# Optimization experiments

Measured on AMD Instinct MI355X. Metric: run time of the kernel, lower is better.

The kernel has to match this reference:

```python
import jax, jax.numpy as jnp
import numpy as np
from jax.scipy.special import gammaln

B, N, F, K = 128, 29, 64, 64
MAXZ, NITER, NPATH = 56, 2, 20
CUTOFF = 5.0


def setup_inputs() -> dict:
    key = jax.random.key(0)
    ks = jax.random.split(key, 16)
    atomic_numbers = jax.random.randint(ks[0], (B, N), 1, MAXZ)
    positions = jax.random.normal(ks[1], (B, N, 3), dtype=jnp.float32) * 2.0
    Ef = jax.random.normal(ks[2], (B, 3), dtype=jnp.float32)
    # fully connected molecular graph (all ordered pairs i != j), E = N*(N-1) = 812
    ii, jj = np.meshgrid(np.arange(N), np.arange(N), indexing="ij")
    m = ii != jj
    dst_idx = jnp.asarray(ii[m], dtype=jnp.int32)
    src_idx = jnp.asarray(jj[m], dtype=jnp.int32)
    s = 1.0 / np.sqrt(F)
    t = 0.2  # tensor-product path weight scale (keeps activations bounded)
    return {
        "atomic_numbers": atomic_numbers, "positions": positions, "Ef": Ef,
        "dst_idx": dst_idx, "src_idx": src_idx,
        "embed": jax.random.normal(ks[3], (MAXZ, F), dtype=jnp.float32) * s,
        "mp_basis_w": jax.random.normal(ks[4], (NITER, K, F), dtype=jnp.float32) / np.sqrt(K),
        "mp_tp_w": jax.random.normal(ks[5], (NITER, NPATH, F), dtype=jnp.float32) * t,
        "d1_w": jax.random.normal(ks[6], (NITER, 2, 2, F, F), dtype=jnp.float32) * s,
        "d1_b": jnp.zeros((NITER, 2, F), dtype=jnp.float32),
        "d2_w": jax.random.normal(ks[7], (NITER, 2, 2, F, F), dtype=jnp.float32) * s,
        "d2_b": jnp.zeros((NITER, 2, F), dtype=jnp.float32),
        "tens_w": jax.random.normal(ks[8], (NITER, NPATH, F), dtype=jnp.float32) * t,
        "td_dense_w": jax.random.normal(ks[9], (NITER, 2, 2, F, F), dtype=jnp.float32) * s,
        "td_tp_w": jax.random.normal(ks[10], (NITER, NPATH, F), dtype=jnp.float32) * t,
        "out_w": jax.random.normal(ks[11], (F,), dtype=jnp.float32) * s,
        "element_bias": jax.random.normal(ks[12], (MAXZ,), dtype=jnp.float32) * 0.1,
    }


def _tp(a, b, w):
    """Channelwise Clebsch-Gordan tensor product for max_degree=1 with parity channels.
    a, b: (M, 2, 4, F) with axis1 = (regular, pseudo), axis2 = (l=0, l=1 x/y/z).
    w: (20, F) learned per-path weights (5 l-paths x 4 parity combos)."""
    M, Fd = a.shape[0], a.shape[-1]
    sr = jnp.zeros((M, Fd), a.dtype); sp = jnp.zeros((M, Fd), a.dtype)
    vr = jnp.zeros((M, 3, Fd), a.dtype); vp = jnp.zeros((M, 3, Fd), a.dtype)
    idx = 0
    for p1 in range(2):
        for p2 in range(2):
            s1 = a[:, p1, 0]; v1 = a[:, p1, 1:4]
            s2 = b[:, p2, 0]; v2 = b[:, p2, 1:4]
            pl0a = 1 - 2 * p1; pl0b = 1 - 2 * p2   # parity of l=0 slot
            pl1a = -(1 - 2 * p1); pl1b = -(1 - 2 * p2)  # parity of l=1 slot
            tt = w[idx] * s1 * s2
            if pl0a * pl0b == 1: sr = sr + tt
            else: sp = sp + tt
            tt = w[idx + 1] * s1[:, None, :] * v2
            if pl0a * pl1b == -1: vr = vr + tt
            else: vp = vp + tt
            tt = w[idx + 2] * v1 * s2[:, None, :]
            if pl1a * pl0b == -1: vr = vr + tt
            else: vp = vp + tt
            tt = w[idx + 3] * jnp.sum(v1 * v2, axis=1)
            if pl1a * pl1b == 1: sr = sr + tt
            else: sp = sp + tt
            tt = w[idx + 4] * jnp.cross(v1, v2, axis=1)
            if pl1a * pl1b == -1: vr = vr + tt
            else: vp = vp + tt
            idx += 5
    reg = jnp.concatenate([sr[:, None, :], vr], axis=1)
    pse = jnp.concatenate([sp[:, None, :], vp], axis=1)
    return jnp.stack([reg, pse], axis=1)  # (M, 2, 4, F)


def _dense(x, W, b=None):
    # per-(parity, degree) linear map over features; W: (2, 2, F, F), b: (2, F)
    s = jnp.einsum("npf,pfg->npg", x[:, :, 0, :], W[:, 0])
    v = jnp.einsum("npdf,pfg->npdg", x[:, :, 1:4, :], W[:, 1])
    if b is not None:
        s = s + b
    return jnp.concatenate([s[:, :, None, :], v], axis=2)


def _silu(x):
    # gated equivariant silu: silu on scalars, sigmoid(scalar) gate on vectors
    s = x[:, :, 0:1, :]
    g = jax.nn.sigmoid(s)
    return jnp.concatenate([s * g, x[:, :, 1:4, :] * g], axis=2)


def _radial(r):
    # reciprocal Bernstein radial basis with smooth cutoff
    k = jnp.arange(K, dtype=r.dtype)
    logc = gammaln(float(K)) - gammaln(k + 1.0) - gammaln(float(K) - k)
    u = 1.0 / (1.0 + r)
    logb = logc + k * jnp.log(u)[:, None] + (K - 1.0 - k) * jnp.log(jnp.maximum(1.0 - u, 1e-12))[:, None]
    x2 = (r / CUTOFF) ** 2
    fcut = jnp.where(x2 < 1.0, jnp.exp(1.0 - 1.0 / jnp.maximum(1.0 - x2, 1e-12)), 0.0)
    return jnp.exp(logb) * fcut[:, None]  # (E, K)


def reference(atomic_numbers, positions, Ef, dst_idx, src_idx, embed, mp_basis_w,
              mp_tp_w, d1_w, d1_b, d2_w, d2_b, tens_w, td_dense_w, td_tp_w,
              out_w, element_bias):
    Bsz, Nn = atomic_numbers.shape
    BN = Bsz * Nn
    Fd = embed.shape[-1]
    pos = positions.reshape(-1, 3)
    Z = atomic_numbers.reshape(-1)
    offsets = (jnp.arange(Bsz, dtype=dst_idx.dtype) * Nn)
    dstf = (dst_idx[None, :] + offsets[:, None]).reshape(-1)  # (B*E,)
    srcf = (src_idx[None, :] + offsets[:, None]).reshape(-1)
    disp = pos[srcf] - pos[dstf]                               # (B*E, 3)
    r = jnp.sqrt(jnp.sum(disp * disp, axis=-1) + 1e-12)
    unit = disp / r[:, None]
    sph = jnp.concatenate([jnp.ones_like(r)[:, None], unit], axis=-1)  # (B*E, 4)
    basis = sph[:, :, None] * _radial(r)[:, None, :]           # (B*E, 4, K)

    x = jnp.zeros((BN, 2, 4, Fd), dtype=positions.dtype)
    x = x.at[:, 0, 0, :].set(embed[Z])

    xEFv = jnp.concatenate([jnp.ones((Bsz, 1), positions.dtype), Ef], axis=-1)  # (B, 4)
    xEF = jnp.repeat(xEFv, Nn, axis=0)                          # (BN, 4)
    xEF = jnp.broadcast_to(xEF[:, None, :, None], (BN, 2, 4, Fd))

    for i in range(NITER):
        bproj = jnp.einsum("edk,kf->edf", basis, mp_basis_w[i])  # (B*E, 4, F)
        bfeat = jnp.stack([bproj, jnp.zeros_like(bproj)], axis=1)  # (B*E, 2, 4, F)
        msg = _tp(x[srcf], bfeat, mp_tp_w[i])
        if i == NITER - 1:  # last iteration: max_degree=0 messages
            msg = msg * jnp.array([1.0, 0.0, 0.0, 0.0], msg.dtype)[None, None, :, None]
        y = jax.ops.segment_sum(msg, dstf, num_segments=BN)
        x = x + y
        h = _dense(x, d1_w[i], d1_b[i])
        h = _silu(h)
        h = _dense(h, d2_w[i], d2_b[i])
        x = h + y
        x = x + _tp(x, xEF, tens_w[i])          # Tensor()(x, xEF)
        x = _tp(x, _dense(x, td_dense_w[i]), td_tp_w[i])  # TensorDense

    s = x[:, 0, 0, :]  # degree-0 regular channel
    atomic_energies = s @ out_w + element_bias[Z]
    energy = atomic_energies.reshape(Bsz, Nn).sum(axis=1)
    return energy
```

## Files before the change

kernel.cpp:

```cpp
#include <hip/hip_runtime.h>

#define NB 128
#define NA 29
#define BN (NB*NA)
#define FD 64


__global__ void prep_kernel(const float* __restrict__ d1b,
                            const float* __restrict__ d2b,
                            const float* __restrict__ d2w,
                            float* __restrict__ logc, float* __restrict__ c4,
                            float* __restrict__ out)
{
  const int t = threadIdx.x;
  if (t < 64) {
    logc[t] = lgammaf(64.0f) - lgammaf((float)t + 1.0f) - lgammaf(64.0f - (float)t);
  } else if (t < 128) {
    const int g = t - 64;
    float acc = d2b[64 + g];
    for (int f = 0; f < 64; ++f) {
      const float v  = d1b[64 + f];
      const float sv = v / (1.0f + expf(-v));
      acc += d2w[2*4096 + f*64 + g] * sv;
    }
    c4[g] = acc;
  } else {
    out[t - 128] = 0.0f;
  }
}

template<bool LAST>
__global__ __launch_bounds__(256) void fmsg_kernel(
    const int*   __restrict__ Z,
    const float* __restrict__ pos,
    const float* __restrict__ src,
    const float* __restrict__ wtp,
    const float* __restrict__ Wb,
    const float* __restrict__ logc_tab,
    float* __restrict__ y)
{
  __shared__ float elu[28], el1mu[28], efc[28];
  __shared__ float us[28][3];
  __shared__ float rads[28][FD];
  __shared__ float emb_sh[NA][FD];
  __shared__ float yred[4][4][FD];
  const int bn = blockIdx.x, b = bn / NA, n = bn - b*NA;
  const int tid = threadIdx.x, lane = tid & 63, wv = tid >> 6;

  if (tid < 28) {
    const int jr = tid, j = jr + (jr >= n ? 1 : 0);
    const float dx = pos[(b*NA+j)*3+0] - pos[(b*NA+n)*3+0];
    const float dy = pos[(b*NA+j)*3+1] - pos[(b*NA+n)*3+1];
    const float dz = pos[(b*NA+j)*3+2] - pos[(b*NA+n)*3+2];
    const float r  = sqrtf(dx*dx + dy*dy + dz*dz + 1e-12f);
    const float ri = 1.0f / r;
    us[jr][0] = dx*ri; us[jr][1] = dy*ri; us[jr][2] = dz*ri;
    const float u  = 1.0f/(1.0f + r);
    elu[jr]   = logf(u);
    el1mu[jr] = logf(fmaxf(1.0f - u, 1e-12f));
    const float x2 = (r*0.2f)*(r*0.2f);
    efc[jr] = (x2 < 1.0f) ? expf(1.0f - 1.0f/fmaxf(1.0f - x2, 1e-12f)) : 0.0f;
  }
  if constexpr (!LAST) {
    for (int idx = tid; idx < NA*FD; idx += 256)
      emb_sh[idx>>6][idx&63] = src[Z[b*NA + (idx>>6)]*FD + (idx&63)];
  }
  const float kk   = (float)lane;
  const float logc = logc_tab[lane];
  __syncthreads();

  #pragma unroll
  for (int i = 0; i < 7; ++i) {
    const int e = wv*7 + i;
    rads[e][lane] = expf(logc + kk*elu[e] + (63.0f - kk)*el1mu[e]) * efc[e];
  }
  float wb[64];
  #pragma unroll
  for (int k = 0; k < 64; ++k) wb[k] = Wb[k*FD + lane];

  float y0 = 0.0f, y1 = 0.0f, y2 = 0.0f, y3 = 0.0f, y4 = 0.0f;
  const float wm0 = wtp[0*FD + lane];
  const float wm1 = LAST ? 0.0f : wtp[1*FD + lane];
  const float wm3 = LAST ? wtp[3*FD + lane]  : 0.0f;
  const float wm5 = LAST ? wtp[10*FD + lane] : 0.0f;
  const float wm8 = LAST ? wtp[13*FD + lane] : 0.0f;

  #pragma unroll
  for (int i = 0; i < 7; ++i) {
    const int jr = wv*7 + i;
    float a0 = 0.0f;
    #pragma unroll
    for (int k4 = 0; k4 < 16; ++k4) {
      const float4 rv = *(const float4*)&rads[jr][k4*4];
      a0 += wb[k4*4+0]*rv.x + wb[k4*4+1]*rv.y + wb[k4*4+2]*rv.z + wb[k4*4+3]*rv.w;
    }
    const int j = jr + (jr >= n ? 1 : 0);
    const float ux = us[jr][0], uy = us[jr][1], uz = us[jr][2];
    if constexpr (!LAST) {
      const float t0 = a0 * emb_sh[j][lane];
      y0 += wm0*t0;
      const float t1 = wm1*t0;
      y1 += t1*ux; y2 += t1*uy; y3 += t1*uz;
    } else {
      const float* xj = src + (size_t)(b*NA + j)*512 + lane;
      const float s1   = xj[0];
      const float dot1 = xj[64]*ux + xj[128]*uy + xj[192]*uz;
      const float s1p  = xj[256];
      const float dotp = xj[320]*ux + xj[384]*uy + xj[448]*uz;
      y0 += a0*(wm0*s1  + wm3*dot1);
      y4 += a0*(wm5*s1p + wm8*dotp);
    }
  }

  if constexpr (!LAST) {
    yred[wv][0][lane] = y0; yred[wv][1][lane] = y1;
    yred[wv][2][lane] = y2; yred[wv][3][lane] = y3;
  } else {
    yred[wv][0][lane] = y0; yred[wv][1][lane] = y4;
  }
  __syncthreads();
  if (wv == 0) {
    if constexpr (!LAST) {
      #pragma unroll
      for (int c = 0; c < 4; ++c) {
        const float s = yred[0][c][lane] + yred[1][c][lane]
                      + yred[2][c][lane] + yred[3][c][lane];
        y[(size_t)bn*256 + c*64 + lane] = s;
      }
    } else {
      const float s0 = yred[0][0][lane] + yred[1][0][lane]
                     + yred[2][0][lane] + yred[3][0][lane];
      const float s4 = yred[0][1][lane] + yred[1][1][lane]
                     + yred[2][1][lane] + yred[3][1][lane];
      y[(size_t)bn*512 + lane]       = s0;
      y[(size_t)bn*512 + 256 + lane] = s4;
    }
  }
}

__device__ __forceinline__ void tp20(const float* a, const float* bb,
                                     const float* w, float* o)
{
  #pragma unroll
  for (int p1 = 0; p1 < 2; ++p1) {
    #pragma unroll
    for (int p2 = 0; p2 < 2; ++p2) {
      const float* w5 = w + 5*(2*p1 + p2);
      const float s1 = a[p1*4+0], x1 = a[p1*4+1], y1 = a[p1*4+2], z1 = a[p1*4+3];
      const float s2 = bb[p2*4+0], x2 = bb[p2*4+1], y2 = bb[p2*4+2], z2 = bb[p2*4+3];
      const int so = (p1 == p2) ? 0 : 4;
      const int vo = 4 - so;
      o[so+0] += w5[0]*(s1*s2) + w5[3]*(x1*x2 + y1*y2 + z1*z2);
      o[so+1] += w5[1]*(s1*x2) + w5[2]*(x1*s2);
      o[so+2] += w5[1]*(s1*y2) + w5[2]*(y1*s2);
      o[so+3] += w5[1]*(s1*z2) + w5[2]*(z1*s2);
      o[vo+1] += w5[4]*(y1*z2 - z1*y2);
      o[vo+2] += w5[4]*(z1*x2 - x1*z2);
      o[vo+3] += w5[4]*(x1*y2 - y1*x2);
    }
  }
}

__device__ __forceinline__ void stage2(float* __restrict__ wst,
                                       const float* __restrict__ src, int tid)
{
  const float4* s = (const float4*)src;
  float4* d = (float4*)wst;
  #pragma unroll
  for (int i = 0; i < 8; ++i) d[tid + i*256] = s[tid + i*256];
}

__device__ __forceinline__ void denseP2(const float* __restrict__ wst,
                                        const float* __restrict__ rA,
                                        const float* __restrict__ rB,
                                        float bs, int g,
                                        float oA[4], float oB[4])
{
  float a0A = bs, a0B = bs;
  #pragma unroll
  for (int f4 = 0; f4 < 16; ++f4) {
    const float w0 = wst[(f4*4+0)*64+g], w1 = wst[(f4*4+1)*64+g];
    const float w2 = wst[(f4*4+2)*64+g], w3 = wst[(f4*4+3)*64+g];
    const float4 xA = *(const float4*)&rA[f4*4];
    const float4 xB = *(const float4*)&rB[f4*4];
    a0A += w0*xA.x + w1*xA.y + w2*xA.z + w3*xA.w;
    a0B += w0*xB.x + w1*xB.y + w2*xB.z + w3*xB.w;
  }
  oA[0] = a0A; oB[0] = a0B;
  float a1A = 0, a2A = 0, a3A = 0, a1B = 0, a2B = 0, a3B = 0;
  #pragma unroll
  for (int f4 = 0; f4 < 16; ++f4) {
    const float w0 = wst[4096+(f4*4+0)*64+g], w1 = wst[4096+(f4*4+1)*64+g];
    const float w2 = wst[4096+(f4*4+2)*64+g], w3 = wst[4096+(f4*4+3)*64+g];
    const float4 aA = *(const float4*)&rA[ 64+f4*4];
    const float4 bA = *(const float4*)&rA[128+f4*4];
    const float4 cA = *(const float4*)&rA[192+f4*4];
    const float4 aB = *(const float4*)&rB[ 64+f4*4];
    const float4 bB = *(const float4*)&rB[128+f4*4];
    const float4 cB = *(const float4*)&rB[192+f4*4];
    a1A += w0*aA.x + w1*aA.y + w2*aA.z + w3*aA.w;
    a2A += w0*bA.x + w1*bA.y + w2*bA.z + w3*bA.w;
    a3A += w0*cA.x + w1*cA.y + w2*cA.z + w3*cA.w;
    a1B += w0*aB.x + w1*aB.y + w2*aB.z + w3*aB.w;
    a2B += w0*bB.x + w1*bB.y + w2*bB.z + w3*bB.w;
    a3B += w0*cB.x + w1*cB.y + w2*cB.z + w3*cB.w;
  }
  oA[1] = a1A; oA[2] = a2A; oA[3] = a3A;
  oB[1] = a1B; oB[2] = a2B; oB[3] = a3B;
}

template<bool LAST>
__global__ __launch_bounds__(256) void node_kernel(
    const int*   __restrict__ Z,
    const float* __restrict__ embed,
    const float* __restrict__ Ef,
    const float* __restrict__ d1w, const float* __restrict__ d1b,
    const float* __restrict__ d2w, const float* __restrict__ d2b,
    const float* __restrict__ tens_w,
    const float* __restrict__ tdw,
    const float* __restrict__ td_tp_w,
    const float* __restrict__ out_w,
    const float* __restrict__ ebias,
    const float* __restrict__ c4,
    const float* __restrict__ xin,
    const float* __restrict__ yin,
    float* __restrict__ xout,
    float* __restrict__ out)
{
  __shared__ float wst[2*64*64];
  __shared__ float row[8][8][FD];
  const int tid = threadIdx.x, r = tid >> 6, g = tid & 63;
  const int ndA = blockIdx.x*8 + r*2, ndB = ndA + 1;
  float* rowA = &row[r*2+0][0][0];
  float* rowB = &row[r*2+1][0][0];

  float yA[4], yB[4];
  float y0A = 0, y4A = 0, y0B = 0, y4B = 0;
  if constexpr (!LAST) {
    #pragma unroll
    for (int c = 0; c < 4; ++c) {
      yA[c] = yin[(size_t)ndA*256 + c*64 + g];
      yB[c] = yin[(size_t)ndB*256 + c*64 + g];
    }
    rowA[g] = embed[Z[ndA]*FD + g] + yA[0];
    rowB[g] = embed[Z[ndB]*FD + g] + yB[0];
    #pragma unroll
    for (int c = 1; c < 4; ++c) { rowA[c*64+g] = yA[c]; rowB[c*64+g] = yB[c]; }
  } else {
    y0A = yin[(size_t)ndA*512 + g];     y4A = yin[(size_t)ndA*512 + 256 + g];
    y0B = yin[(size_t)ndB*512 + g];     y4B = yin[(size_t)ndB*512 + 256 + g];
    #pragma unroll
    for (int pc = 0; pc < 8; ++pc) {
      float vA = xin[(size_t)ndA*512 + pc*64 + g];
      float vB = xin[(size_t)ndB*512 + pc*64 + g];
      if (pc == 0) { vA += y0A; vB += y0B; }
      if (pc == 4) { vA += y4A; vB += y4B; }
      rowA[pc*64+g] = vA; rowB[pc*64+g] = vB;
    }
  }
  stage2(wst, d1w, tid);
  __syncthreads();

  {
    float hA[4], hB[4];
    denseP2(wst, rowA, rowB, d1b[g], g, hA, hB);
    const float sA = 1.0f/(1.0f + expf(-hA[0]));
    const float sB = 1.0f/(1.0f + expf(-hB[0]));
    rowA[g] = hA[0]*sA; rowB[g] = hB[0]*sB;
    #pragma unroll
    for (int c = 1; c < 4; ++c) { rowA[c*64+g] = hA[c]*sA; rowB[c*64+g] = hB[c]*sB; }
  }
  __syncthreads();
  if constexpr (LAST) {
    stage2(wst, d1w + 8192, tid);
    __syncthreads();
    float hA[4], hB[4];
    denseP2(wst, rowA + 256, rowB + 256, d1b[64+g], g, hA, hB);
    const float sA = 1.0f/(1.0f + expf(-hA[0]));
    const float sB = 1.0f/(1.0f + expf(-hB[0]));
    rowA[256+g] = hA[0]*sA; rowB[256+g] = hB[0]*sB;
    #pragma unroll
    for (int c = 1; c < 4; ++c) { rowA[256+c*64+g] = hA[c]*sA; rowB[256+c*64+g] = hB[c]*sB; }
    __syncthreads();
  }
  stage2(wst, d2w, tid);
  __syncthreads();

  float x2A[8], x2B[8];
  {
    float oA[4], oB[4];
    denseP2(wst, rowA, rowB, d2b[g], g, oA, oB);
    #pragma unroll
    for (int c = 0; c < 4; ++c) { x2A[c] = oA[c]; x2B[c] = oB[c]; }
  }
  if constexpr (!LAST) {
    #pragma unroll
    for (int c = 0; c < 4; ++c) { x2A[c] += yA[c]; x2B[c] += yB[c]; }
    const float c4v = c4[g];
    x2A[4] = c4v; x2B[4] = c4v;
    x2A[5] = x2A[6] = x2A[7] = 0.0f;
    x2B[5] = x2B[6] = x2B[7] = 0.0f;
  } else {
    x2A[0] += y0A; x2B[0] += y0B;
    __syncthreads();
    stage2(wst, d2w + 8192, tid);
    __syncthreads();
    float oA[4], oB[4];
    denseP2(wst, rowA + 256, rowB + 256, d2b[64+g], g, oA, oB);
    x2A[4] = oA[0] + y4A; x2A[5] = oA[1]; x2A[6] = oA[2]; x2A[7] = oA[3];
    x2B[4] = oB[0] + y4B; x2B[5] = oB[1]; x2B[6] = oB[2]; x2B[7] = oB[3];
  }

  float x3A[8], x3B[8];
  {
    float w20[20];
    #pragma unroll
    for (int q = 0; q < 20; ++q) w20[q] = tens_w[q*FD + g];
    const int bA = ndA / NA, bB = ndB / NA;
    {
      const float bbv[8] = {1.0f, Ef[bA*3+0], Ef[bA*3+1], Ef[bA*3+2],
                            1.0f, Ef[bA*3+0], Ef[bA*3+1], Ef[bA*3+2]};
      float o[8] = {0,0,0,0,0,0,0,0};
      tp20(x2A, bbv, w20, o);
      #pragma unroll
      for (int pc = 0; pc < 8; ++pc) { x3A[pc] = x2A[pc] + o[pc]; rowA[pc*64+g] = x3A[pc]; }
    }
    {
      const float bbv[8] = {1.0f, Ef[bB*3+0], Ef[bB*3+1], Ef[bB*3+2],
                            1.0f, Ef[bB*3+0], Ef[bB*3+1], Ef[bB*3+2]};
      float o[8] = {0,0,0,0,0,0,0,0};
      tp20(x2B, bbv, w20, o);
      #pragma unroll
      for (int pc = 0; pc < 8; ++pc) { x3B[pc] = x2B[pc] + o[pc]; rowB[pc*64+g] = x3B[pc]; }
    }
  }
  __syncthreads();
  stage2(wst, tdw, tid);
  __syncthreads();

  float tdA[8], tdB[8];
  {
    float oA[4], oB[4];
    denseP2(wst, rowA, rowB, 0.0f, g, oA, oB);
    #pragma unroll
    for (int c = 0; c < 4; ++c) { tdA[c] = oA[c]; tdB[c] = oB[c]; }
  }
  __syncthreads();
  stage2(wst, tdw + 8192, tid);
  __syncthreads();
  {
    float oA[4], oB[4];
    denseP2(wst, rowA + 256, rowB + 256, 0.0f, g, oA, oB);
    #pragma unroll
    for (int c = 0; c < 4; ++c) { tdA[4+c] = oA[c]; tdB[4+c] = oB[c]; }
  }

  if constexpr (LAST) {
    const float wa = td_tp_w[0*FD+g],  wb = td_tp_w[3*FD+g];
    const float wc = td_tp_w[15*FD+g], wd = td_tp_w[18*FD+g];
    const float ow = out_w[g];
    float pA = ow * (wa*(x3A[0]*tdA[0])
                   + wb*(x3A[1]*tdA[1] + x3A[2]*tdA[2] + x3A[3]*tdA[3])
                   + wc*(x3A[4]*tdA[4])
                   + wd*(x3A[5]*tdA[5] + x3A[6]*tdA[6] + x3A[7]*tdA[7]));
    float pB = ow * (wa*(x3B[0]*tdB[0])
                   + wb*(x3B[1]*tdB[1] + x3B[2]*tdB[2] + x3B[3]*tdB[3])
                   + wc*(x3B[4]*tdB[4])
                   + wd*(x3B[5]*tdB[5] + x3B[6]*tdB[6] + x3B[7]*tdB[7]));
    #pragma unroll
    for (int off = 32; off > 0; off >>= 1) {
      pA += __shfl_xor(pA, off, 64);
      pB += __shfl_xor(pB, off, 64);
    }
    if (g == 0) {
      atomicAdd(&out[ndA/NA], pA + ebias[Z[ndA]]);
      atomicAdd(&out[ndB/NA], pB + ebias[Z[ndB]]);
    }
  } else {
    float w20[20];
    #pragma unroll
    for (int q = 0; q < 20; ++q) w20[q] = td_tp_w[q*FD + g];
    {
      float o[8] = {0,0,0,0,0,0,0,0};
      tp20(x3A, tdA, w20, o);
      #pragma unroll
      for (int pc = 0; pc < 8; ++pc) xout[(size_t)ndA*512 + pc*64 + g] = o[pc];
    }
    {
      float o[8] = {0,0,0,0,0,0,0,0};
      tp20(x3B, tdB, w20, o);
      #pragma unroll
      for (int pc = 0; pc < 8; ++pc) xout[(size_t)ndB*512 + pc*64 + g] = o[pc];
    }
  }
}

extern "C" void kernel_launch(void* const* d_in, const int* in_sizes, int n_in,
                              void* d_out, int out_size, void* d_ws, size_t ws_size,
                              hipStream_t stream)
{
  (void)in_sizes; (void)n_in; (void)out_size; (void)ws_size;
  const int*   Z     = (const int*)  d_in[0];
  const float* pos   = (const float*)d_in[1];
  const float* Ef    = (const float*)d_in[2];
  const float* embed = (const float*)d_in[5];
  const float* mpbw  = (const float*)d_in[6];
  const float* mptpw = (const float*)d_in[7];
  const float* d1w   = (const float*)d_in[8];
  const float* d1b   = (const float*)d_in[9];
  const float* d2w   = (const float*)d_in[10];
  const float* d2b   = (const float*)d_in[11];
  const float* tensw = (const float*)d_in[12];
  const float* tdw   = (const float*)d_in[13];
  const float* tdtpw = (const float*)d_in[14];
  const float* outw  = (const float*)d_in[15];
  const float* ebias = (const float*)d_in[16];
  float* out = (float*)d_out;

  float* logc = (float*)d_ws;
  float* c4   = logc + 64;
  float* xg   = c4 + 64;
  float* yg   = xg + (size_t)BN*512;

  prep_kernel<<<1, 256, 0, stream>>>(d1b, d2b, d2w, logc, c4, out);
  fmsg_kernel<false><<<BN, 256, 0, stream>>>(Z, pos, embed, mptpw, mpbw, logc, yg);
  node_kernel<false><<<BN/8, 256, 0, stream>>>(Z, embed, Ef,
      d1w, d1b, d2w, d2b, tensw, tdw, tdtpw, outw, ebias, c4,
      nullptr, yg, xg, nullptr);
  fmsg_kernel<true><<<BN, 256, 0, stream>>>(Z, pos, xg, mptpw + 1280,
      mpbw + 4096, logc, yg);
  node_kernel<true><<<BN/8, 256, 0, stream>>>(Z, embed, Ef,
      d1w + 16384, d1b + 128, d2w + 16384, d2b + 128, tensw + 1280,
      tdw + 16384, tdtpw + 1280, outw, ebias, c4,
      xg, yg, nullptr, out);
}
```

Measured before the change: 124.4 us.

## Fuse message and node phases into one persistent kernel per iteration

Merges the per-edge message kernel and the per-node update kernel into a single kernel per iteration. Each of 464 blocks serially computes messages for 8 nodes, keeps them in shared memory, then runs the node update on those same nodes. The prep kernel is also folded in: the lgamma table and the constant vector are recomputed inside each block. This removes the global round trip of the message buffer and three kernel launches. In exchange, message-phase parallelism drops from one block per node to 464 blocks looping serially, and the larger shared-memory footprint lowers occupancy.

```diff
diff --git a/kernel.cpp b/kernel.cpp
--- a/kernel.cpp
+++ b/kernel.cpp
@@ -4,139 +4,8 @@
 #define NA 29
 #define BN (NB*NA)
 #define FD 64
-
-
-__global__ void prep_kernel(const float* __restrict__ d1b,
-                            const float* __restrict__ d2b,
-                            const float* __restrict__ d2w,
-                            float* __restrict__ logc, float* __restrict__ c4,
-                            float* __restrict__ out)
-{
-  const int t = threadIdx.x;
-  if (t < 64) {
-    logc[t] = lgammaf(64.0f) - lgammaf((float)t + 1.0f) - lgammaf(64.0f - (float)t);
-  } else if (t < 128) {
-    const int g = t - 64;
-    float acc = d2b[64 + g];
-    for (int f = 0; f < 64; ++f) {
-      const float v  = d1b[64 + f];
-      const float sv = v / (1.0f + expf(-v));
-      acc += d2w[2*4096 + f*64 + g] * sv;
-    }
-    c4[g] = acc;
-  } else {
-    out[t - 128] = 0.0f;
-  }
-}
-
-template<bool LAST>
-__global__ __launch_bounds__(256) void fmsg_kernel(
-    const int*   __restrict__ Z,
-    const float* __restrict__ pos,
-    const float* __restrict__ src,
-    const float* __restrict__ wtp,
-    const float* __restrict__ Wb,
-    const float* __restrict__ logc_tab,
-    float* __restrict__ y)
-{
-  __shared__ float elu[28], el1mu[28], efc[28];
-  __shared__ float us[28][3];
-  __shared__ float rads[28][FD];
-  __shared__ float emb_sh[NA][FD];
-  __shared__ float yred[4][4][FD];
-  const int bn = blockIdx.x, b = bn / NA, n = bn - b*NA;
-  const int tid = threadIdx.x, lane = tid & 63, wv = tid >> 6;
-
-  if (tid < 28) {
-    const int jr = tid, j = jr + (jr >= n ? 1 : 0);
-    const float dx = pos[(b*NA+j)*3+0] - pos[(b*NA+n)*3+0];
-    const float dy = pos[(b*NA+j)*3+1] - pos[(b*NA+n)*3+1];
-    const float dz = pos[(b*NA+j)*3+2] - pos[(b*NA+n)*3+2];
-    const float r  = sqrtf(dx*dx + dy*dy + dz*dz + 1e-12f);
-    const float ri = 1.0f / r;
-    us[jr][0] = dx*ri; us[jr][1] = dy*ri; us[jr][2] = dz*ri;
-    const float u  = 1.0f/(1.0f + r);
-    elu[jr]   = logf(u);
-    el1mu[jr] = logf(fmaxf(1.0f - u, 1e-12f));
-    const float x2 = (r*0.2f)*(r*0.2f);
-    efc[jr] = (x2 < 1.0f) ? expf(1.0f - 1.0f/fmaxf(1.0f - x2, 1e-12f)) : 0.0f;
-  }
-  if constexpr (!LAST) {
-    for (int idx = tid; idx < NA*FD; idx += 256)
-      emb_sh[idx>>6][idx&63] = src[Z[b*NA + (idx>>6)]*FD + (idx&63)];
-  }
-  const float kk   = (float)lane;
-  const float logc = logc_tab[lane];
-  __syncthreads();
-
-  #pragma unroll
-  for (int i = 0; i < 7; ++i) {
-    const int e = wv*7 + i;
-    rads[e][lane] = expf(logc + kk*elu[e] + (63.0f - kk)*el1mu[e]) * efc[e];
-  }
-  float wb[64];
-  #pragma unroll
-  for (int k = 0; k < 64; ++k) wb[k] = Wb[k*FD + lane];
-
-  float y0 = 0.0f, y1 = 0.0f, y2 = 0.0f, y3 = 0.0f, y4 = 0.0f;
-  const float wm0 = wtp[0*FD + lane];
-  const float wm1 = LAST ? 0.0f : wtp[1*FD + lane];
-  const float wm3 = LAST ? wtp[3*FD + lane]  : 0.0f;
-  const float wm5 = LAST ? wtp[10*FD + lane] : 0.0f;
-  const float wm8 = LAST ? wtp[13*FD + lane] : 0.0f;
-
-  #pragma unroll
-  for (int i = 0; i < 7; ++i) {
-    const int jr = wv*7 + i;
-    float a0 = 0.0f;
-    #pragma unroll
-    for (int k4 = 0; k4 < 16; ++k4) {
-      const float4 rv = *(const float4*)&rads[jr][k4*4];
-      a0 += wb[k4*4+0]*rv.x + wb[k4*4+1]*rv.y + wb[k4*4+2]*rv.z + wb[k4*4+3]*rv.w;
-    }
-    const int j = jr + (jr >= n ? 1 : 0);
-    const float ux = us[jr][0], uy = us[jr][1], uz = us[jr][2];
-    if constexpr (!LAST) {
-      const float t0 = a0 * emb_sh[j][lane];
-      y0 += wm0*t0;
-      const float t1 = wm1*t0;
-      y1 += t1*ux; y2 += t1*uy; y3 += t1*uz;
-    } else {
-      const float* xj = src + (size_t)(b*NA + j)*512 + lane;
-      const float s1   = xj[0];
-      const float dot1 = xj[64]*ux + xj[128]*uy + xj[192]*uz;
-      const float s1p  = xj[256];
-      const float dotp = xj[320]*ux + xj[384]*uy + xj[448]*uz;
-      y0 += a0*(wm0*s1  + wm3*dot1);
-      y4 += a0*(wm5*s1p + wm8*dotp);
-    }
-  }
-
-  if constexpr (!LAST) {
-    yred[wv][0][lane] = y0; yred[wv][1][lane] = y1;
-    yred[wv][2][lane] = y2; yred[wv][3][lane] = y3;
-  } else {
-    yred[wv][0][lane] = y0; yred[wv][1][lane] = y4;
-  }
-  __syncthreads();
-  if (wv == 0) {
-    if constexpr (!LAST) {
-      #pragma unroll
-      for (int c = 0; c < 4; ++c) {
-        const float s = yred[0][c][lane] + yred[1][c][lane]
-                      + yred[2][c][lane] + yred[3][c][lane];
-        y[(size_t)bn*256 + c*64 + lane] = s;
-      }
-    } else {
-      const float s0 = yred[0][0][lane] + yred[1][0][lane]
-                     + yred[2][0][lane] + yred[3][0][lane];
-      const float s4 = yred[0][1][lane] + yred[1][1][lane]
-                     + yred[2][1][lane] + yred[3][1][lane];
-      y[(size_t)bn*512 + lane]       = s0;
-      y[(size_t)bn*512 + 256 + lane] = s4;
-    }
-  }
-}
+#define NBLK 464
+
 
 __device__ __forceinline__ void tp20(const float* a, const float* bb,
                                      const float* w, float* o)
@@ -210,49 +79,142 @@
 }
 
 template<bool LAST>
-__global__ __launch_bounds__(256) void node_kernel(
-    const int*   __restrict__ Z,
-    const float* __restrict__ embed,
+__device__ __forceinline__ void fmsg_phase(
+    float* __restrict__ ov, float (*y_sh)[4][FD],
+    const int* __restrict__ Z, const float* __restrict__ pos,
+    const float* __restrict__ src,
+    const float* __restrict__ wtp, const float* __restrict__ Wb,
+    float logc, int j, int tid, int lane, int wv)
+{
+  float* rads  = ov;
+  float* emb   = ov + 1792;
+  float* yred  = ov + 3648;
+  float* elu   = ov + 4672;
+  float* el1mu = ov + 4700;
+  float* efc   = ov + 4728;
+  float* us    = ov + 4756;
+  const float kk = (float)lane;
+
+  float wb[64];
+  #pragma unroll
+  for (int k = 0; k < 64; ++k) wb[k] = Wb[k*FD + lane];
+  const float wm0 = wtp[0*FD + lane];
+  const float wm1 = LAST ? 0.0f : wtp[1*FD + lane];
+  const float wm3 = LAST ? wtp[3*FD + lane]  : 0.0f;
+  const float wm5 = LAST ? wtp[10*FD + lane] : 0.0f;
+  const float wm8 = LAST ? wtp[13*FD + lane] : 0.0f;
+
+  for (int t = 0; t < 8; ++t) {
+    const int bn = j + NBLK*t;
+    const int b = bn / NA, n = bn - b*NA;
+    __syncthreads();
+    if (tid < 28) {
+      const int jr = tid, jj = jr + (jr >= n ? 1 : 0);
+      const float dx = pos[(b*NA+jj)*3+0] - pos[(b*NA+n)*3+0];
+      const float dy = pos[(b*NA+jj)*3+1] - pos[(b*NA+n)*3+1];
+      const float dz = pos[(b*NA+jj)*3+2] - pos[(b*NA+n)*3+2];
+      const float r  = sqrtf(dx*dx + dy*dy + dz*dz + 1e-12f);
+      const float ri = 1.0f / r;
+      us[jr*3+0] = dx*ri; us[jr*3+1] = dy*ri; us[jr*3+2] = dz*ri;
+      const float u = 1.0f/(1.0f + r);
+      elu[jr]   = logf(u);
+      el1mu[jr] = logf(fmaxf(1.0f - u, 1e-12f));
+      const float x2 = (r*0.2f)*(r*0.2f);
+      efc[jr] = (x2 < 1.0f) ? expf(1.0f - 1.0f/fmaxf(1.0f - x2, 1e-12f)) : 0.0f;
+    }
+    if constexpr (!LAST) {
+      for (int idx = tid; idx < NA*FD; idx += 256)
+        emb[idx] = src[Z[b*NA + (idx>>6)]*FD + (idx&63)];
+    }
+    __syncthreads();
+
+    #pragma unroll
+    for (int i = 0; i < 7; ++i) {
+      const int e = wv*7 + i;
+      rads[e*64 + lane] = expf(logc + kk*elu[e] + (63.0f - kk)*el1mu[e]) * efc[e];
+    }
+    float y0 = 0.0f, y1 = 0.0f, y2 = 0.0f, y3 = 0.0f, y4 = 0.0f;
+    #pragma unroll
+    for (int i = 0; i < 7; ++i) {
+      const int jr = wv*7 + i;
+      float a0 = 0.0f;
+      #pragma unroll
+      for (int k4 = 0; k4 < 16; ++k4) {
+        const float4 rv = *(const float4*)&rads[jr*64 + k4*4];
+        a0 += wb[k4*4+0]*rv.x + wb[k4*4+1]*rv.y + wb[k4*4+2]*rv.z + wb[k4*4+3]*rv.w;
+      }
+      const int jj = jr + (jr >= n ? 1 : 0);
+      const float ux = us[jr*3+0], uy = us[jr*3+1], uz = us[jr*3+2];
+      if constexpr (!LAST) {
+        const float t0 = a0 * emb[jj*64 + lane];
+        y0 += wm0*t0;
+        const float t1 = wm1*t0;
+        y1 += t1*ux; y2 += t1*uy; y3 += t1*uz;
+      } else {
+        const float* xj = src + (size_t)(b*NA + jj)*512 + lane;
+        const float s1   = xj[0];
+        const float dot1 = xj[64]*ux + xj[128]*uy + xj[192]*uz;
+        const float s1p  = xj[256];
+        const float dotp = xj[320]*ux + xj[384]*uy + xj[448]*uz;
+        y0 += a0*(wm0*s1  + wm3*dot1);
+        y4 += a0*(wm5*s1p + wm8*dotp);
+      }
+    }
+    if constexpr (!LAST) {
+      yred[(wv*4+0)*64+lane] = y0; yred[(wv*4+1)*64+lane] = y1;
+      yred[(wv*4+2)*64+lane] = y2; yred[(wv*4+3)*64+lane] = y3;
+    } else {
+      yred[(wv*4+0)*64+lane] = y0; yred[(wv*4+1)*64+lane] = y4;
+    }
+    __syncthreads();
+    if (wv == 0) {
+      const int nch = LAST ? 2 : 4;
+      for (int c = 0; c < nch; ++c) {
+        y_sh[t][c][lane] = yred[(0*4+c)*64+lane] + yred[(1*4+c)*64+lane]
+                         + yred[(2*4+c)*64+lane] + yred[(3*4+c)*64+lane];
+      }
+    }
+  }
+  __syncthreads();
+}
+
+template<bool LAST>
+__device__ __forceinline__ void node_phase(
+    float* __restrict__ ov, float (*y_sh)[4][FD],
+    const float* __restrict__ c4_sh,
+    const int* __restrict__ Z, const float* __restrict__ embed,
     const float* __restrict__ Ef,
     const float* __restrict__ d1w, const float* __restrict__ d1b,
     const float* __restrict__ d2w, const float* __restrict__ d2b,
-    const float* __restrict__ tens_w,
-    const float* __restrict__ tdw,
-    const float* __restrict__ td_tp_w,
-    const float* __restrict__ out_w,
+    const float* __restrict__ tens_w, const float* __restrict__ tdw,
+    const float* __restrict__ td_tp_w, const float* __restrict__ out_w,
     const float* __restrict__ ebias,
-    const float* __restrict__ c4,
-    const float* __restrict__ xin,
-    const float* __restrict__ yin,
-    float* __restrict__ xout,
-    float* __restrict__ out)
-{
-  __shared__ float wst[2*64*64];
-  __shared__ float row[8][8][FD];
-  const int tid = threadIdx.x, r = tid >> 6, g = tid & 63;
-  const int ndA = blockIdx.x*8 + r*2, ndB = ndA + 1;
-  float* rowA = &row[r*2+0][0][0];
-  float* rowB = &row[r*2+1][0][0];
+    float* __restrict__ xg, float* __restrict__ out, int j, int tid)
+{
+  float* wst  = ov;
+  float* rows = ov + 8192;
+  const int r = tid >> 6, g = tid & 63;
+  const int iA = 2*r, iB = iA + 1;
+  const int ndA = j + NBLK*iA, ndB = j + NBLK*iB;
+  float* rowA = rows + iA*512;
+  float* rowB = rows + iB*512;
 
   float yA[4], yB[4];
   float y0A = 0, y4A = 0, y0B = 0, y4B = 0;
   if constexpr (!LAST) {
     #pragma unroll
-    for (int c = 0; c < 4; ++c) {
-      yA[c] = yin[(size_t)ndA*256 + c*64 + g];
-      yB[c] = yin[(size_t)ndB*256 + c*64 + g];
-    }
+    for (int c = 0; c < 4; ++c) { yA[c] = y_sh[iA][c][g]; yB[c] = y_sh[iB][c][g]; }
     rowA[g] = embed[Z[ndA]*FD + g] + yA[0];
     rowB[g] = embed[Z[ndB]*FD + g] + yB[0];
     #pragma unroll
     for (int c = 1; c < 4; ++c) { rowA[c*64+g] = yA[c]; rowB[c*64+g] = yB[c]; }
   } else {
-    y0A = yin[(size_t)ndA*512 + g];     y4A = yin[(size_t)ndA*512 + 256 + g];
-    y0B = yin[(size_t)ndB*512 + g];     y4B = yin[(size_t)ndB*512 + 256 + g];
+    y0A = y_sh[iA][0][g]; y4A = y_sh[iA][1][g];
+    y0B = y_sh[iB][0][g]; y4B = y_sh[iB][1][g];
     #pragma unroll
     for (int pc = 0; pc < 8; ++pc) {
-      float vA = xin[(size_t)ndA*512 + pc*64 + g];
-      float vB = xin[(size_t)ndB*512 + pc*64 + g];
+      float vA = xg[(size_t)ndA*512 + pc*64 + g];
+      float vB = xg[(size_t)ndB*512 + pc*64 + g];
       if (pc == 0) { vA += y0A; vB += y0B; }
       if (pc == 4) { vA += y4A; vB += y4B; }
       rowA[pc*64+g] = vA; rowB[pc*64+g] = vB;
@@ -296,7 +258,7 @@
   if constexpr (!LAST) {
     #pragma unroll
     for (int c = 0; c < 4; ++c) { x2A[c] += yA[c]; x2B[c] += yB[c]; }
-    const float c4v = c4[g];
+    const float c4v = c4_sh[g];
     x2A[4] = c4v; x2B[4] = c4v;
     x2A[5] = x2A[6] = x2A[7] = 0.0f;
     x2B[5] = x2B[6] = x2B[7] = 0.0f;
@@ -384,15 +346,60 @@
       float o[8] = {0,0,0,0,0,0,0,0};
       tp20(x3A, tdA, w20, o);
       #pragma unroll
-      for (int pc = 0; pc < 8; ++pc) xout[(size_t)ndA*512 + pc*64 + g] = o[pc];
+      for (int pc = 0; pc < 8; ++pc) xg[(size_t)ndA*512 + pc*64 + g] = o[pc];
     }
     {
       float o[8] = {0,0,0,0,0,0,0,0};
       tp20(x3B, tdB, w20, o);
       #pragma unroll
-      for (int pc = 0; pc < 8; ++pc) xout[(size_t)ndB*512 + pc*64 + g] = o[pc];
-    }
-  }
+      for (int pc = 0; pc < 8; ++pc) xg[(size_t)ndB*512 + pc*64 + g] = o[pc];
+    }
+  }
+}
+
+template<bool LAST>
+__global__ __launch_bounds__(256) void iter_kernel(
+    const int*   __restrict__ Z,
+    const float* __restrict__ pos,
+    const float* __restrict__ Ef,
+    const float* __restrict__ embed,
+    const float* __restrict__ mpbw,
+    const float* __restrict__ mptpw,
+    const float* __restrict__ d1w, const float* __restrict__ d1b,
+    const float* __restrict__ d2w, const float* __restrict__ d2b,
+    const float* __restrict__ tensw,
+    const float* __restrict__ tdw,
+    const float* __restrict__ tdtpw,
+    const float* __restrict__ outw,
+    const float* __restrict__ ebias,
+    float* __restrict__ xg,
+    float* __restrict__ out)
+{
+  __shared__ float4 ovb[3072];
+  __shared__ float y_sh[8][4][FD];
+  __shared__ float c4_sh[FD];
+  float* ov = (float*)ovb;
+
+  const int j = blockIdx.x, tid = threadIdx.x, lane = tid & 63, wv = tid >> 6;
+  const float kk = (float)lane;
+  const float logc = lgammaf(64.0f) - lgammaf(kk + 1.0f) - lgammaf(64.0f - kk);
+
+  if constexpr (!LAST) {
+    if (j < NB && tid == 0) out[j] = 0.0f;
+    float* sil = ov;
+    if (tid < 64) { const float v = d1b[64+tid]; sil[tid] = v/(1.0f + expf(-v)); }
+    __syncthreads();
+    if (tid < 64) {
+      float acc = d2b[64 + tid];
+      for (int f = 0; f < 64; ++f) acc += d2w[8192 + f*64 + tid] * sil[f];
+      c4_sh[tid] = acc;
+    }
+  }
+
+  const float* src = LAST ? xg : embed;
+  fmsg_phase<LAST>(ov, y_sh, Z, pos, src, mptpw, mpbw, logc, j, tid, lane, wv);
+  node_phase<LAST>(ov, y_sh, c4_sh, Z, embed, Ef, d1w, d1b, d2w, d2b,
+                   tensw, tdw, tdtpw, outw, ebias, xg, out, j, tid);
 }
 
 extern "C" void kernel_launch(void* const* d_in, const int* in_sizes, int n_in,
@@ -416,21 +423,13 @@
   const float* outw  = (const float*)d_in[15];
   const float* ebias = (const float*)d_in[16];
   float* out = (float*)d_out;
-
-  float* logc = (float*)d_ws;
-  float* c4   = logc + 64;
-  float* xg   = c4 + 64;
-  float* yg   = xg + (size_t)BN*512;
-
-  prep_kernel<<<1, 256, 0, stream>>>(d1b, d2b, d2w, logc, c4, out);
-  fmsg_kernel<false><<<BN, 256, 0, stream>>>(Z, pos, embed, mptpw, mpbw, logc, yg);
-  node_kernel<false><<<BN/8, 256, 0, stream>>>(Z, embed, Ef,
-      d1w, d1b, d2w, d2b, tensw, tdw, tdtpw, outw, ebias, c4,
-      nullptr, yg, xg, nullptr);
-  fmsg_kernel<true><<<BN, 256, 0, stream>>>(Z, pos, xg, mptpw + 1280,
-      mpbw + 4096, logc, yg);
-  node_kernel<true><<<BN/8, 256, 0, stream>>>(Z, embed, Ef,
-      d1w + 16384, d1b + 128, d2w + 16384, d2b + 128, tensw + 1280,
-      tdw + 16384, tdtpw + 1280, outw, ebias, c4,
-      xg, yg, nullptr, out);
-}
+  float* xg  = (float*)d_ws;
+
+  iter_kernel<false><<<NBLK, 256, 0, stream>>>(Z, pos, Ef, embed,
+      mpbw, mptpw, d1w, d1b, d2w, d2b, tensw, tdw, tdtpw, outw, ebias,
+      xg, out);
+  iter_kernel<true><<<NBLK, 256, 0, stream>>>(Z, pos, Ef, embed,
+      mpbw + 4096, mptpw + 1280, d1w + 16384, d1b + 128, d2w + 16384,
+      d2b + 128, tensw + 1280, tdw + 16384, tdtpw + 1280, outw, ebias,
+      xg, out);
+}
```

Measured after the change: 131.0 us. 5.4% more time.
